# Optimization experiments

Hardware: AMD Instinct MI355X
Metric: run time of the kernel (lower is better)

Reference implementation:

```python
import jax, jax.numpy as jnp
import numpy as np

EPS = 1e-12  # F.normalize eps
NUM_CLASSES = 80


def _l2_normalize(x, axis):
    # matches torch F.normalize: x / max(||x||_2, eps)
    n = jnp.sqrt(jnp.sum(x * x, axis=axis, keepdims=True))
    return x / jnp.maximum(n, EPS)


def setup_inputs() -> dict:
    key = jax.random.key(0)
    k1, k2, k3, k4 = jax.random.split(key, 4)
    B, C, H, W = 16, 256, 128, 128
    N = NUM_CLASSES
    features = jax.random.normal(k1, (B, C, H, W), dtype=jnp.float32)
    centroids = jax.random.normal(k2, (N, C), dtype=jnp.float32)
    fc_w = jax.random.normal(k3, (C, C, 1, 1), dtype=jnp.float32) * 0.02
    fc_b = jax.random.normal(k4, (C,), dtype=jnp.float32) * 0.01
    return {"features": features, "centroids": centroids, "fc_w": fc_w, "fc_b": fc_b}


def reference(features, centroids, fc_w, fc_b):
    N = centroids.shape[0]
    # cosine similarity to class centroids: [B, N, H, W]
    sim = jnp.einsum('bchw,nc->bnhw', _l2_normalize(features, axis=1),
                     _l2_normalize(centroids, axis=1))
    # hard one-hot assignment along class dim (scatter of argmax)
    idx = jnp.argmax(sim, axis=1)                              # [B, H, W]
    mask = jax.nn.one_hot(idx, N, axis=1, dtype=features.dtype)  # [B, N, H, W]
    # per-image, per-class mean feature (gather/blend)
    sum_x = jnp.einsum('bnhw,bchw->bnc', mask, features)       # [B, N, C]
    count = jnp.sum(mask, axis=(2, 3))[:, :, None]             # [B, N, 1]
    cent = sum_x / jnp.maximum(count, 1.0)
    delta = jnp.einsum('bnhw,bnc->bchw', mask, cent) - features
    alpha = jnp.exp(-jnp.mean(jnp.square(delta), axis=1, keepdims=True))  # [B,1,H,W]
    x = features + alpha * delta
    # 1x1 conv == channel matmul
    out = jnp.einsum('bchw,oc->bohw', x, fc_w[:, :, 0, 0]) + fc_b[None, :, None, None]
    return jax.nn.relu(out)
```

## Files before the change

kernel.cpp:

```cpp
#include <hip/hip_runtime.h>


typedef __bf16 bf16x8 __attribute__((ext_vector_type(8)));
typedef float  f32x4  __attribute__((ext_vector_type(4)));
typedef unsigned char u8;

__device__ __forceinline__ unsigned short f2b(float f) {
  unsigned u = __float_as_uint(f);
  return (unsigned short)((u + 0x7fffu + ((u >> 16) & 1u)) >> 16);
}
__device__ __forceinline__ float b2f(unsigned short s) {
  return __uint_as_float((unsigned)s << 16);
}

__global__ __launch_bounds__(256) void k0_cnorm(const float* __restrict__ cent,
                                                float* __restrict__ cnT,
                                                int* __restrict__ cntg) {
  int n = blockIdx.x, t = threadIdx.x;
  if (t < 16) cntg[n * 16 + t] = 0;
  float v = cent[n * 256 + t];
  float s = v * v;
  #pragma unroll
  for (int o = 32; o > 0; o >>= 1) s += __shfl_down(s, o, 64);
  __shared__ float red[4];
  if ((t & 63) == 0) red[t >> 6] = s;
  __syncthreads();
  float tot = red[0] + red[1] + red[2] + red[3];
  float dn = fmaxf(sqrtf(tot), 1e-12f);
  cnT[t * 80 + n] = v / dn;
}

__global__ __launch_bounds__(256) void k0_wprep(const float* __restrict__ fcw,
                                                unsigned short* __restrict__ wks,
                                                float* __restrict__ wt) {
  int o = blockIdx.x, c = threadIdx.x;
  float w = fcw[o * 256 + c];
  wt[c * 256 + o] = w;
  wks[((c >> 5) * 256 + o) * 32 + (c & 31)] = f2b(w);
}

__global__ __launch_bounds__(256, 4) void k1f(const float* __restrict__ feat,
                                              const float* __restrict__ cnT,
                                              u8* __restrict__ idxb,
                                              float* __restrict__ fsqg,
                                              int* __restrict__ cntg,
                                              float* __restrict__ part) {
  __shared__ alignas(8) u8 idxl[256];
  __shared__ int lh[80];
  const int b = blockIdx.x >> 6, chunk = blockIdx.x & 63;
  const int px0 = chunk << 8;
  const int t = threadIdx.x, wv = t >> 6, ln = t & 63, lo = ln & 15, hi = ln >> 4;
  if (t < 80) lh[t] = 0;
  __syncthreads();

  const int pi = px0 | t;
  const float* fb = feat + (size_t)b * 256 * 16384 + pi;
  float best, fsq; int bi;
  {
    float g[40];
    #pragma unroll
    for (int n = 0; n < 40; ++n) g[n] = 0.f;
    fsq = 0.f;
    #pragma unroll 4
    for (int c = 0; c < 256; ++c) {
      float v = fb[(size_t)c * 16384];
      fsq = fmaf(v, v, fsq);
      const float* cr = cnT + c * 80;
      #pragma unroll
      for (int n = 0; n < 40; ++n) g[n] = fmaf(v, cr[n], g[n]);
    }
    best = g[0]; bi = 0;
    #pragma unroll
    for (int n = 1; n < 40; ++n) if (g[n] > best) { best = g[n]; bi = n; }
  }
  {
    float g[40];
    #pragma unroll
    for (int n = 0; n < 40; ++n) g[n] = 0.f;
    #pragma unroll 4
    for (int c = 0; c < 256; ++c) {
      float v = fb[(size_t)c * 16384];
      const float* cr = cnT + c * 80 + 40;
      #pragma unroll
      for (int n = 0; n < 40; ++n) g[n] = fmaf(v, cr[n], g[n]);
    }
    float b2 = g[0]; int i2 = 40;
    #pragma unroll
    for (int n = 1; n < 40; ++n) if (g[n] > b2) { b2 = g[n]; i2 = 40 + n; }
    if (b2 > best) { best = b2; bi = i2; }
  }
  idxb[b * 16384 + pi] = (u8)bi;
  fsqg[b * 16384 + pi] = fsq;
  idxl[t] = (u8)bi;
  atomicAdd(&lh[bi], 1);
  __syncthreads();
  if (t < 80) atomicAdd(&cntg[b * 80 + t], lh[t]);

  const int chb = wv * 64;
  float* pb = part + ((size_t)(b * 64 + chunk) * 80) * 256;
  #pragma unroll 1
  for (int half = 0; half < 2; ++half) {
    f32x4 acc[5][2];
    f32x4 zz = {0.f, 0.f, 0.f, 0.f};
    #pragma unroll
    for (int mt = 0; mt < 5; ++mt) { acc[mt][0] = zz; acc[mt][1] = zz; }
    #pragma unroll 2
    for (int ks = 0; ks < 8; ++ks) {
      uint2 iv = *(const uint2*)&idxl[ks * 32 + hi * 8];
      int id[8];
      #pragma unroll
      for (int j = 0; j < 4; ++j) { id[j] = (iv.x >> (8 * j)) & 255; id[4 + j] = (iv.y >> (8 * j)) & 255; }
      bf16x8 bfr[2];
      #pragma unroll
      for (int n2 = 0; n2 < 2; ++n2) {
        int nt = half * 2 + n2;
        const float* bp = feat + ((size_t)b * 256 + chb + nt * 16 + lo) * 16384 + px0 + ks * 32 + hi * 8;
        float4 v0 = *(const float4*)bp;
        float4 v1 = *(const float4*)(bp + 4);
        union { unsigned short u[8]; bf16x8 v; } bb;
        bb.u[0] = f2b(v0.x); bb.u[1] = f2b(v0.y); bb.u[2] = f2b(v0.z); bb.u[3] = f2b(v0.w);
        bb.u[4] = f2b(v1.x); bb.u[5] = f2b(v1.y); bb.u[6] = f2b(v1.z); bb.u[7] = f2b(v1.w);
        bfr[n2] = bb.v;
      }
      #pragma unroll
      for (int mt = 0; mt < 5; ++mt) {
        int row = mt * 16 + lo;
        union { unsigned short u[8]; bf16x8 v; } ma;
        #pragma unroll
        for (int j = 0; j < 8; ++j) ma.u[j] = (id[j] == row) ? (unsigned short)0x3F80 : (unsigned short)0;
        #pragma unroll
        for (int n2 = 0; n2 < 2; ++n2)
          acc[mt][n2] = __builtin_amdgcn_mfma_f32_16x16x32_bf16(ma.v, bfr[n2], acc[mt][n2], 0, 0, 0);
      }
    }
    #pragma unroll
    for (int mt = 0; mt < 5; ++mt)
      #pragma unroll
      for (int n2 = 0; n2 < 2; ++n2)
        #pragma unroll
        for (int r = 0; r < 4; ++r)
          pb[(mt * 16 + hi * 4 + r) * 256 + chb + (half * 2 + n2) * 16 + lo] = acc[mt][n2][r];
  }
}

__global__ __launch_bounds__(256) void k2_cent(const float* __restrict__ part,
                                               const int* __restrict__ cntg,
                                               const float* __restrict__ wt,
                                               unsigned short* __restrict__ centf,
                                               float* __restrict__ csqg,
                                               float* __restrict__ chatg) {
  int bn = blockIdx.x; int b = bn / 80, n = bn - b * 80; int t = threadIdx.x;
  float dn = fmaxf((float)cntg[bn], 1.0f);
  float s = 0.f;
  const float* pp = part + ((size_t)(b * 64) * 80 + n) * 256 + t;
  #pragma unroll 8
  for (int ck = 0; ck < 64; ++ck) s += pp[(size_t)ck * 80 * 256];
  float cv = s / dn;
  __shared__ float cl[256];
  __shared__ float red[4];
  cl[t] = cv;
  centf[(size_t)bn * 256 + t] = f2b(cv);
  float q = cv * cv;
  #pragma unroll
  for (int o = 32; o > 0; o >>= 1) q += __shfl_down(q, o, 64);
  if ((t & 63) == 0) red[t >> 6] = q;
  __syncthreads();
  if (t == 0) csqg[bn] = red[0] + red[1] + red[2] + red[3];
  float acc = 0.f;
  #pragma unroll 4
  for (int c = 0; c < 256; ++c) acc = fmaf(wt[c * 256 + t], cl[c], acc);
  chatg[(size_t)bn * 256 + t] = acc;
}

__global__ __launch_bounds__(512) void k3b_gemm(const float* __restrict__ feat,
    const u8* __restrict__ idxb, const float* __restrict__ fsqg,
    const float* __restrict__ csqg, const unsigned short* __restrict__ centf,
    const float* __restrict__ chatg, const unsigned short* __restrict__ wks,
    const float* __restrict__ fcb, float* __restrict__ out) {
  __shared__ alignas(16) unsigned short featT[2][64 * 264];
  __shared__ float alphal[64];
  __shared__ int cidl[64];
  const int t = threadIdx.x;
  const int w = t >> 6, ln = t & 63, lo = ln & 15, hi = ln >> 4;
  const int pl = ln, cph = w;

  bf16x8 wf[2][8];
  #pragma unroll
  for (int ml = 0; ml < 2; ++ml)
    #pragma unroll
    for (int ks = 0; ks < 8; ++ks)
      wf[ml][ks] = *(const bf16x8*)&wks[((size_t)ks * 256 + (w * 2 + ml) * 16 + lo) * 32 + hi * 8];
  f32x4 bias2[2];
  #pragma unroll
  for (int ml = 0; ml < 2; ++ml)
    bias2[ml] = *(const f32x4*)&fcb[w * 32 + ml * 16 + hi * 4];

  const int tile0 = blockIdx.x * 8;
  {
    int b = tile0 >> 8, p0 = (tile0 & 255) << 6;
    const float* fb = feat + ((size_t)b * 256 + cph * 32) * 16384 + p0 + pl;
    #pragma unroll
    for (int jj = 0; jj < 4; ++jj) {
      union { unsigned short u[8]; uint4 q; } pk;
      #pragma unroll
      for (int e = 0; e < 8; ++e) pk.u[e] = f2b(fb[(size_t)(jj * 8 + e) * 16384]);
      *(uint4*)&featT[0][pl * 264 + cph * 32 + jj * 8] = pk.q;
    }
  }

  float nxv[32];
  for (int rep = 0; rep < 8; ++rep) {
    const int cur = rep & 1;
    const int tile = tile0 + rep;
    const int b = tile >> 8, p0 = (tile & 255) << 6;

    __syncthreads();

    if (rep < 7) {
      int t2 = tile + 1;
      int b2 = t2 >> 8, p02 = (t2 & 255) << 6;
      const float* fb2 = feat + ((size_t)b2 * 256 + cph * 32) * 16384 + p02 + pl;
      #pragma unroll
      for (int e = 0; e < 32; ++e) nxv[e] = fb2[(size_t)e * 16384];
    }

    {
      int p = t >> 3, sub = t & 7;
      int cid = idxb[b * 16384 + p0 + p];
      const unsigned short* cw = centf + ((size_t)b * 80 + cid) * 256 + sub * 32;
      const unsigned short* fr = &featT[cur][p * 264 + sub * 32];
      float sel = 0.f;
      #pragma unroll
      for (int j = 0; j < 4; ++j) {
        uint4 cc = *(const uint4*)&cw[j * 8];
        uint4 ff = *(const uint4*)&fr[j * 8];
        sel = fmaf(b2f((unsigned short)(ff.x & 0xffff)), b2f((unsigned short)(cc.x & 0xffff)), sel);
        sel = fmaf(b2f((unsigned short)(ff.x >> 16)),    b2f((unsigned short)(cc.x >> 16)),    sel);
        sel = fmaf(b2f((unsigned short)(ff.y & 0xffff)), b2f((unsigned short)(cc.y & 0xffff)), sel);
        sel = fmaf(b2f((unsigned short)(ff.y >> 16)),    b2f((unsigned short)(cc.y >> 16)),    sel);
        sel = fmaf(b2f((unsigned short)(ff.z & 0xffff)), b2f((unsigned short)(cc.z & 0xffff)), sel);
        sel = fmaf(b2f((unsigned short)(ff.z >> 16)),    b2f((unsigned short)(cc.z >> 16)),    sel);
        sel = fmaf(b2f((unsigned short)(ff.w & 0xffff)), b2f((unsigned short)(cc.w & 0xffff)), sel);
        sel = fmaf(b2f((unsigned short)(ff.w >> 16)),    b2f((unsigned short)(cc.w >> 16)),    sel);
      }
      sel += __shfl_xor(sel, 1, 64);
      sel += __shfl_xor(sel, 2, 64);
      sel += __shfl_xor(sel, 4, 64);
      if (sub == 0) {
        float fsq = fsqg[b * 16384 + p0 + p];
        float msq = (csqg[b * 80 + cid] - 2.f * sel + fsq) * (1.f / 256.f);
        alphal[p] = expf(-msq);
        cidl[p] = cid;
      }
    }

    f32x4 acc[2][4];
    f32x4 zz = {0.f, 0.f, 0.f, 0.f};
    #pragma unroll
    for (int ml = 0; ml < 2; ++ml)
      #pragma unroll
      for (int pt = 0; pt < 4; ++pt) acc[ml][pt] = zz;

    #pragma unroll
    for (int ks = 0; ks < 8; ++ks) {
      bf16x8 bfr[4];
      #pragma unroll
      for (int pt = 0; pt < 4; ++pt)
        bfr[pt] = *(const bf16x8*)&featT[cur][(pt * 16 + lo) * 264 + ks * 32 + hi * 8];
      #pragma unroll
      for (int ml = 0; ml < 2; ++ml)
        #pragma unroll
        for (int pt = 0; pt < 4; ++pt)
          acc[ml][pt] = __builtin_amdgcn_mfma_f32_16x16x32_bf16(wf[ml][ks], bfr[pt], acc[ml][pt], 0, 0, 0);
    }
    __syncthreads();

    #pragma unroll
    for (int pt = 0; pt < 4; ++pt) {
      int plx = pt * 16 + lo;
      int p = p0 + plx;
      float a = alphal[plx];
      float om = 1.f - a;
      const float* crow = chatg + ((size_t)b * 80 + cidl[plx]) * 256;
      #pragma unroll
      for (int ml = 0; ml < 2; ++ml) {
        int o0 = w * 32 + ml * 16 + hi * 4;
        float4 c4 = *(const float4*)&crow[o0];
        size_t ob = ((size_t)b * 256 + o0) * 16384 + p;
        out[ob            ] = fmaxf(fmaf(a, c4.x, om * acc[ml][pt][0]) + bias2[ml][0], 0.f);
        out[ob + 16384    ] = fmaxf(fmaf(a, c4.y, om * acc[ml][pt][1]) + bias2[ml][1], 0.f);
        out[ob + 2 * 16384] = fmaxf(fmaf(a, c4.z, om * acc[ml][pt][2]) + bias2[ml][2], 0.f);
        out[ob + 3 * 16384] = fmaxf(fmaf(a, c4.w, om * acc[ml][pt][3]) + bias2[ml][3], 0.f);
      }
    }

    if (rep < 7) {
      #pragma unroll
      for (int jj = 0; jj < 4; ++jj) {
        union { unsigned short u[8]; uint4 q; } pk;
        #pragma unroll
        for (int e = 0; e < 8; ++e) pk.u[e] = f2b(nxv[jj * 8 + e]);
        *(uint4*)&featT[cur ^ 1][pl * 264 + cph * 32 + jj * 8] = pk.q;
      }
    }
  }
}

extern "C" void kernel_launch(void* const* d_in, const int* in_sizes, int n_in,
                              void* d_out, int out_size, void* d_ws, size_t ws_size,
                              hipStream_t stream) {
  (void)in_sizes; (void)n_in; (void)out_size; (void)ws_size;
  const float* feat = (const float*)d_in[0];
  const float* cent = (const float*)d_in[1];
  const float* fcw  = (const float*)d_in[2];
  const float* fcb  = (const float*)d_in[3];
  float* out = (float*)d_out;
  char* ws = (char*)d_ws;
  float* cnT             = (float*)(ws);
  float* wt              = (float*)(ws + 81920);
  unsigned short* wks    = (unsigned short*)(ws + 344064);
  unsigned short* centf  = (unsigned short*)(ws + 475136);
  u8*    idxb            = (u8*)(ws + 1130496);
  float* fsq             = (float*)(ws + 1392640);
  int*   cntg            = (int*)(ws + 2441216);
  float* csq             = (float*)(ws + 2446336);
  float* chat            = (float*)(ws + 2451456);
  float* part            = (float*)(ws + 3762176);

  k0_cnorm<<<80, 256, 0, stream>>>(cent, cnT, cntg);
  k0_wprep<<<256, 256, 0, stream>>>(fcw, wks, wt);
  k1f<<<1024, 256, 0, stream>>>(feat, cnT, idxb, fsq, cntg, part);
  k2_cent<<<1280, 256, 0, stream>>>(part, cntg, wt, centf, csq, chat);
  k3b_gemm<<<512, 512, 0, stream>>>(feat, idxb, fsq, csq, centf, chat, wks, fcb, out);
}
```

Before: 389.9 us.

## Process two pixels per thread in argmax kernel and halve block count

Each thread in the similarity/argmax kernel now handles two adjacent pixels with float2 loads and packed FMAs, so every centroid value read is reused across two pixels. The grid shrinks from 1024 to 512 blocks, each covering 512 pixels, and the per-chunk partial-sum buffer and its reduction in the centroid kernel are resized to match. In exchange, register pressure doubles for the 40-wide accumulators, which risks spills or lower occupancy, and there are fewer blocks to spread across the GPU.

Measured after the change: 562.9 us. 44.4% more time.

```diff
diff --git a/kernel.cpp b/kernel.cpp
--- a/kernel.cpp
+++ b/kernel.cpp
@@ -3,6 +3,7 @@
 
 typedef __bf16 bf16x8 __attribute__((ext_vector_type(8)));
 typedef float  f32x4  __attribute__((ext_vector_type(4)));
+typedef float  f32x2  __attribute__((ext_vector_type(2)));
 typedef unsigned char u8;
 
 __device__ __forceinline__ unsigned short f2b(float f) {
@@ -45,59 +46,77 @@
                                               float* __restrict__ fsqg,
                                               int* __restrict__ cntg,
                                               float* __restrict__ part) {
-  __shared__ alignas(8) u8 idxl[256];
+  __shared__ alignas(8) u8 idxl[512];
   __shared__ int lh[80];
-  const int b = blockIdx.x >> 6, chunk = blockIdx.x & 63;
-  const int px0 = chunk << 8;
+  const int b = blockIdx.x >> 5, chunk = blockIdx.x & 31;
+  const int px0 = chunk << 9;
   const int t = threadIdx.x, wv = t >> 6, ln = t & 63, lo = ln & 15, hi = ln >> 4;
   if (t < 80) lh[t] = 0;
   __syncthreads();
 
-  const int pi = px0 | t;
-  const float* fb = feat + (size_t)b * 256 * 16384 + pi;
-  float best, fsq; int bi;
+  const int pi0 = px0 | (t << 1);
+  const float* fb = feat + (size_t)b * 256 * 16384 + pi0;
+  float bA, bB, fsA, fsB; int iA, iB;
   {
-    float g[40];
-    #pragma unroll
-    for (int n = 0; n < 40; ++n) g[n] = 0.f;
-    fsq = 0.f;
+    f32x2 g[40];
+    #pragma unroll
+    for (int n = 0; n < 40; ++n) g[n] = (f32x2){0.f, 0.f};
+    f32x2 fs2 = {0.f, 0.f};
     #pragma unroll 4
     for (int c = 0; c < 256; ++c) {
-      float v = fb[(size_t)c * 16384];
-      fsq = fmaf(v, v, fsq);
+      f32x2 v = *(const f32x2*)(fb + (size_t)c * 16384);
+      fs2 = __builtin_elementwise_fma(v, v, fs2);
       const float* cr = cnT + c * 80;
       #pragma unroll
-      for (int n = 0; n < 40; ++n) g[n] = fmaf(v, cr[n], g[n]);
-    }
-    best = g[0]; bi = 0;
-    #pragma unroll
-    for (int n = 1; n < 40; ++n) if (g[n] > best) { best = g[n]; bi = n; }
+      for (int n = 0; n < 40; ++n) {
+        f32x2 cv = {cr[n], cr[n]};
+        g[n] = __builtin_elementwise_fma(v, cv, g[n]);
+      }
+    }
+    fsA = fs2.x; fsB = fs2.y;
+    bA = g[0].x; iA = 0; bB = g[0].y; iB = 0;
+    #pragma unroll
+    for (int n = 1; n < 40; ++n) {
+      if (g[n].x > bA) { bA = g[n].x; iA = n; }
+      if (g[n].y > bB) { bB = g[n].y; iB = n; }
+    }
   }
   {
-    float g[40];
-    #pragma unroll
-    for (int n = 0; n < 40; ++n) g[n] = 0.f;
+    f32x2 g[40];
+    #pragma unroll
+    for (int n = 0; n < 40; ++n) g[n] = (f32x2){0.f, 0.f};
     #pragma unroll 4
     for (int c = 0; c < 256; ++c) {
-      float v = fb[(size_t)c * 16384];
+      f32x2 v = *(const f32x2*)(fb + (size_t)c * 16384);
       const float* cr = cnT + c * 80 + 40;
       #pragma unroll
-      for (int n = 0; n < 40; ++n) g[n] = fmaf(v, cr[n], g[n]);
-    }
-    float b2 = g[0]; int i2 = 40;
-    #pragma unroll
-    for (int n = 1; n < 40; ++n) if (g[n] > b2) { b2 = g[n]; i2 = 40 + n; }
-    if (b2 > best) { best = b2; bi = i2; }
-  }
-  idxb[b * 16384 + pi] = (u8)bi;
-  fsqg[b * 16384 + pi] = fsq;
-  idxl[t] = (u8)bi;
-  atomicAdd(&lh[bi], 1);
+      for (int n = 0; n < 40; ++n) {
+        f32x2 cv = {cr[n], cr[n]};
+        g[n] = __builtin_elementwise_fma(v, cv, g[n]);
+      }
+    }
+    float b2A = g[0].x; int i2A = 40;
+    float b2B = g[0].y; int i2B = 40;
+    #pragma unroll
+    for (int n = 1; n < 40; ++n) {
+      if (g[n].x > b2A) { b2A = g[n].x; i2A = 40 + n; }
+      if (g[n].y > b2B) { b2B = g[n].y; i2B = 40 + n; }
+    }
+    if (b2A > bA) { bA = b2A; iA = i2A; }
+    if (b2B > bB) { bB = b2B; iB = i2B; }
+  }
+  idxb[b * 16384 + pi0] = (u8)iA;
+  idxb[b * 16384 + pi0 + 1] = (u8)iB;
+  *(f32x2*)&fsqg[b * 16384 + pi0] = (f32x2){fsA, fsB};
+  idxl[t << 1] = (u8)iA;
+  idxl[(t << 1) | 1] = (u8)iB;
+  atomicAdd(&lh[iA], 1);
+  atomicAdd(&lh[iB], 1);
   __syncthreads();
   if (t < 80) atomicAdd(&cntg[b * 80 + t], lh[t]);
 
   const int chb = wv * 64;
-  float* pb = part + ((size_t)(b * 64 + chunk) * 80) * 256;
+  float* pb = part + ((size_t)(b * 32 + chunk) * 80) * 256;
   #pragma unroll 1
   for (int half = 0; half < 2; ++half) {
     f32x4 acc[5][2];
@@ -105,7 +124,7 @@
     #pragma unroll
     for (int mt = 0; mt < 5; ++mt) { acc[mt][0] = zz; acc[mt][1] = zz; }
     #pragma unroll 2
-    for (int ks = 0; ks < 8; ++ks) {
+    for (int ks = 0; ks < 16; ++ks) {
       uint2 iv = *(const uint2*)&idxl[ks * 32 + hi * 8];
       int id[8];
       #pragma unroll
@@ -152,9 +171,9 @@
   int bn = blockIdx.x; int b = bn / 80, n = bn - b * 80; int t = threadIdx.x;
   float dn = fmaxf((float)cntg[bn], 1.0f);
   float s = 0.f;
-  const float* pp = part + ((size_t)(b * 64) * 80 + n) * 256 + t;
+  const float* pp = part + ((size_t)(b * 32) * 80 + n) * 256 + t;
   #pragma unroll 8
-  for (int ck = 0; ck < 64; ++ck) s += pp[(size_t)ck * 80 * 256];
+  for (int ck = 0; ck < 32; ++ck) s += pp[(size_t)ck * 80 * 256];
   float cv = s / dn;
   __shared__ float cl[256];
   __shared__ float red[4];
@@ -329,7 +348,7 @@
 
   k0_cnorm<<<80, 256, 0, stream>>>(cent, cnT, cntg);
   k0_wprep<<<256, 256, 0, stream>>>(fcw, wks, wt);
-  k1f<<<1024, 256, 0, stream>>>(feat, cnT, idxb, fsq, cntg, part);
+  k1f<<<512, 256, 0, stream>>>(feat, cnT, idxb, fsq, cntg, part);
   k2_cent<<<1280, 256, 0, stream>>>(part, cntg, wt, centf, csq, chat);
   k3b_gemm<<<512, 512, 0, stream>>>(feat, idxb, fsq, csq, centf, chat, wks, fcb, out);
 }
```

## Split assignment kernel into two variants trading register use for occupancy

Applied to the files above, without the earlier changes.

Splits the per-pixel centroid-assignment kernel into two launches, each covering half of the pixel chunks. The first half uses a new variant with 8 blocks per CU that computes the 80 class similarities in four passes of 20 accumulators, re-reading the feature column for each pass. The second half keeps the original 40-accumulator variant at 4 blocks per CU. The aim is to see whether higher occupancy hides memory latency better than the extra feature reloads cost; the split launch looks experimental.

Result: slower. 728.5 us (+86.8%).

```diff
diff --git a/kernel.cpp b/kernel.cpp
--- a/kernel.cpp
+++ b/kernel.cpp
@@ -39,15 +39,112 @@
   wks[((c >> 5) * 256 + o) * 32 + (c & 31)] = f2b(w);
 }
 
-__global__ __launch_bounds__(256, 4) void k1f(const float* __restrict__ feat,
-                                              const float* __restrict__ cnT,
-                                              u8* __restrict__ idxb,
-                                              float* __restrict__ fsqg,
-                                              int* __restrict__ cntg,
-                                              float* __restrict__ part) {
+__global__ __launch_bounds__(256, 8) void k1f_v8(const float* __restrict__ feat,
+                                                 const float* __restrict__ cnT,
+                                                 u8* __restrict__ idxb,
+                                                 float* __restrict__ fsqg,
+                                                 int* __restrict__ cntg,
+                                                 float* __restrict__ part,
+                                                 int cbase) {
   __shared__ alignas(8) u8 idxl[256];
   __shared__ int lh[80];
-  const int b = blockIdx.x >> 6, chunk = blockIdx.x & 63;
+  const int b = blockIdx.x >> 5, chunk = cbase + (blockIdx.x & 31);
+  const int px0 = chunk << 8;
+  const int t = threadIdx.x, wv = t >> 6, ln = t & 63, lo = ln & 15, hi = ln >> 4;
+  if (t < 80) lh[t] = 0;
+  __syncthreads();
+
+  const int pi = px0 | t;
+  const float* fb = feat + (size_t)b * 256 * 16384 + pi;
+  float best, fsq; int bi;
+  {
+    float g[20];
+    #pragma unroll
+    for (int n = 0; n < 20; ++n) g[n] = 0.f;
+    fsq = 0.f;
+    #pragma unroll 4
+    for (int c = 0; c < 256; ++c) {
+      float v = fb[(size_t)c * 16384];
+      fsq = fmaf(v, v, fsq);
+      const float* cr = cnT + c * 80;
+      #pragma unroll
+      for (int n = 0; n < 20; ++n) g[n] = fmaf(v, cr[n], g[n]);
+    }
+    best = g[0]; bi = 0;
+    #pragma unroll
+    for (int n = 1; n < 20; ++n) if (g[n] > best) { best = g[n]; bi = n; }
+  }
+  #pragma unroll 1
+  for (int q = 1; q < 4; ++q) {
+    float g[20];
+    #pragma unroll
+    for (int n = 0; n < 20; ++n) g[n] = 0.f;
+    #pragma unroll 4
+    for (int c = 0; c < 256; ++c) {
+      float v = fb[(size_t)c * 16384];
+      const float* cr = cnT + c * 80 + q * 20;
+      #pragma unroll
+      for (int n = 0; n < 20; ++n) g[n] = fmaf(v, cr[n], g[n]);
+    }
+    float bq = g[0]; int iq = q * 20;
+    #pragma unroll
+    for (int n = 1; n < 20; ++n) if (g[n] > bq) { bq = g[n]; iq = q * 20 + n; }
+    if (bq > best) { best = bq; bi = iq; }
+  }
+  idxb[b * 16384 + pi] = (u8)bi;
+  fsqg[b * 16384 + pi] = fsq;
+  idxl[t] = (u8)bi;
+  atomicAdd(&lh[bi], 1);
+  __syncthreads();
+  if (t < 80) atomicAdd(&cntg[b * 80 + t], lh[t]);
+
+  const int chb = wv * 64;
+  float* pb = part + ((size_t)(b * 64 + chunk) * 80) * 256;
+  #pragma unroll 1
+  for (int qt = 0; qt < 4; ++qt) {
+    f32x4 acc[5];
+    f32x4 zz = {0.f, 0.f, 0.f, 0.f};
+    #pragma unroll
+    for (int mt = 0; mt < 5; ++mt) acc[mt] = zz;
+    #pragma unroll 2
+    for (int ks = 0; ks < 8; ++ks) {
+      uint2 iv = *(const uint2*)&idxl[ks * 32 + hi * 8];
+      int id[8];
+      #pragma unroll
+      for (int j = 0; j < 4; ++j) { id[j] = (iv.x >> (8 * j)) & 255; id[4 + j] = (iv.y >> (8 * j)) & 255; }
+      const float* bp = feat + ((size_t)b * 256 + chb + qt * 16 + lo) * 16384 + px0 + ks * 32 + hi * 8;
+      float4 v0 = *(const float4*)bp;
+      float4 v1 = *(const float4*)(bp + 4);
+      union { unsigned short u[8]; bf16x8 v; } bb;
+      bb.u[0] = f2b(v0.x); bb.u[1] = f2b(v0.y); bb.u[2] = f2b(v0.z); bb.u[3] = f2b(v0.w);
+      bb.u[4] = f2b(v1.x); bb.u[5] = f2b(v1.y); bb.u[6] = f2b(v1.z); bb.u[7] = f2b(v1.w);
+      #pragma unroll
+      for (int mt = 0; mt < 5; ++mt) {
+        int row = mt * 16 + lo;
+        union { unsigned short u[8]; bf16x8 v; } ma;
+        #pragma unroll
+        for (int j = 0; j < 8; ++j) ma.u[j] = (id[j] == row) ? (unsigned short)0x3F80 : (unsigned short)0;
+        acc[mt] = __builtin_amdgcn_mfma_f32_16x16x32_bf16(ma.v, bb.v, acc[mt], 0, 0, 0);
+      }
+    }
+    #pragma unroll
+    for (int mt = 0; mt < 5; ++mt)
+      #pragma unroll
+      for (int r = 0; r < 4; ++r)
+        pb[(mt * 16 + hi * 4 + r) * 256 + chb + qt * 16 + lo] = acc[mt][r];
+  }
+}
+
+__global__ __launch_bounds__(256, 4) void k1f_v4(const float* __restrict__ feat,
+                                                 const float* __restrict__ cnT,
+                                                 u8* __restrict__ idxb,
+                                                 float* __restrict__ fsqg,
+                                                 int* __restrict__ cntg,
+                                                 float* __restrict__ part,
+                                                 int cbase) {
+  __shared__ alignas(8) u8 idxl[256];
+  __shared__ int lh[80];
+  const int b = blockIdx.x >> 5, chunk = cbase + (blockIdx.x & 31);
   const int px0 = chunk << 8;
   const int t = threadIdx.x, wv = t >> 6, ln = t & 63, lo = ln & 15, hi = ln >> 4;
   if (t < 80) lh[t] = 0;
@@ -329,7 +426,8 @@
 
   k0_cnorm<<<80, 256, 0, stream>>>(cent, cnT, cntg);
   k0_wprep<<<256, 256, 0, stream>>>(fcw, wks, wt);
-  k1f<<<1024, 256, 0, stream>>>(feat, cnT, idxb, fsq, cntg, part);
+  k1f_v8<<<512, 256, 0, stream>>>(feat, cnT, idxb, fsq, cntg, part, 0);
+  k1f_v4<<<512, 256, 0, stream>>>(feat, cnT, idxb, fsq, cntg, part, 32);
   k2_cent<<<1280, 256, 0, stream>>>(part, cntg, wt, centf, csq, chat);
   k3b_gemm<<<512, 512, 0, stream>>>(feat, idxb, fsq, csq, centf, chat, wks, fcb, out);
 }
```
